# Kernel optimization log

Measured on AMD Instinct MI355X. Metric: run time of the kernel, lower is better.

Reference implementation:

```python
import jax, jax.numpy as jnp
import numpy as np
import math

SCALES = (1, 2, 4)
GROUPS = 8
EPS = 1e-5
TEMPERATURE = 1.0


def bilinear_resize(x, out_h, out_w):
    # torch F.interpolate mode='bilinear', align_corners=False
    B, C, h, w = x.shape
    def coords(out, in_):
        c = (jnp.arange(out, dtype=x.dtype) + 0.5) * (in_ / out) - 0.5
        c = jnp.clip(c, 0.0, in_ - 1.0)
        i0 = jnp.floor(c).astype(jnp.int32)
        i1 = jnp.minimum(i0 + 1, in_ - 1)
        t = c - i0.astype(x.dtype)
        return i0, i1, t
    y0, y1, ty = coords(out_h, h)
    x0, x1, tx = coords(out_w, w)
    r0 = x[:, :, y0, :]
    r1 = x[:, :, y1, :]
    v00 = r0[:, :, :, x0]; v01 = r0[:, :, :, x1]
    v10 = r1[:, :, :, x0]; v11 = r1[:, :, :, x1]
    top = v00 * (1.0 - tx) + v01 * tx
    bot = v10 * (1.0 - tx) + v11 * tx
    return top * (1.0 - ty)[:, None] + bot * ty[:, None]


def group_norm(x, gamma, beta):
    B, C, H, W = x.shape
    xg = x.reshape(B, GROUPS, C // GROUPS, H, W)
    mu = xg.mean(axis=(2, 3, 4), keepdims=True)
    var = xg.var(axis=(2, 3, 4), keepdims=True)
    xn = ((xg - mu) * jax.lax.rsqrt(var + EPS)).reshape(B, C, H, W)
    return xn * gamma[None, :, None, None] + beta[None, :, None, None]


def setup_inputs() -> dict:
    key = jax.random.key(0)
    B, C, H, W = 4, 128, 64, 64
    inter = max(C // 4, 8)  # 32
    S = len(SCALES)
    ks = jax.random.split(key, 8)
    def xavier(k, shape, fan_in, fan_out):
        a = math.sqrt(6.0 / (fan_in + fan_out))
        return jax.random.uniform(k, shape, jnp.float32, -a, a)
    inp = {
        'x': jax.random.normal(ks[0], (B, C, H, W), jnp.float32),
        'gn_w': jnp.ones((S, C), jnp.float32),
        'gn_b': jnp.zeros((S, C), jnp.float32),
        'qw': xavier(ks[1], (S, inter, C), C, inter),
        'qb': jnp.zeros((S, inter), jnp.float32),
        'kw': xavier(ks[2], (S, inter, C), C, inter),
        'kb': jnp.zeros((S, inter), jnp.float32),
        'vw': xavier(ks[3], (S, inter, C), C, inter),
        'vb': jnp.zeros((S, inter), jnp.float32),
        'ow': xavier(ks[4], (S, C, inter), inter, C),
        'ob': jnp.zeros((S, C), jnp.float32),
        'gamma': jnp.full((S,), 0.1 / S, jnp.float32),
        'scale_weights': jnp.full((S,), 1.0 / S, jnp.float32),
    }
    return inp


def _forward(x, gn_w, gn_b, qw, qb, kw, kb, vw, vb, ow, ob, gamma, scale_weights):
    B, C, H, W = x.shape
    inter = qw.shape[1]
    inv_scale = 1.0 / (TEMPERATURE * math.sqrt(inter))
    outs = []
    for i, s in enumerate(SCALES):
        if s == 1:
            xs = x
        else:
            xs = x.reshape(B, C, H // s, s, W // s, s).mean(axis=(3, 5))
        h, w = xs.shape[2], xs.shape[3]
        N = h * w
        xn = group_norm(xs, gn_w[i], gn_b[i])
        # 1x1 convs as channel contractions
        q = (jnp.einsum('oc,bchw->bohw', qw[i], xn) + qb[i][None, :, None, None]).reshape(B, inter, N)
        k = (jnp.einsum('oc,bchw->bohw', kw[i], xn) + kb[i][None, :, None, None]).reshape(B, inter, N)
        v = (jnp.einsum('oc,bchw->bohw', vw[i], xn) + vb[i][None, :, None, None]).reshape(B, inter, N)
        logits = jnp.einsum('bin,bim->bnm', q, k) * inv_scale  # [B, N, N]
        attn = jax.nn.softmax(logits, axis=-1)
        att = jnp.einsum('bnm,bim->bin', attn, v).reshape(B, inter, h, w)
        o = jnp.einsum('ci,bihw->bchw', ow[i], att) + ob[i][None, :, None, None]
        y = gamma[i] * o + xs
        if s > 1:
            y = bilinear_resize(y, H, W)
        outs.append(y)
    wts = jax.nn.softmax(scale_weights, axis=0)
    fused = wts[0] * outs[0]
    for i in range(1, len(outs)):
        fused = fused + wts[i] * outs[i]
    return fused


def reference(x, gn_w, gn_b, qw, qb, kw, kb, vw, vb, ow, ob, gamma, scale_weights):
    return _forward(x, gn_w, gn_b, qw, qb, kw, kb, vw, vb, ow, ob, gamma, scale_weights)
```

## Files before the change

### kernel.cpp

```cpp
#include <hip/hip_runtime.h>
#include <math.h>

#define B 4
#define C 128
#define G 8
#define CPG 16
#define INTER 32
#define SPLIT 16
#define KS 4

#define N1 4096
#define N2 1024
#define N4 256

#define QOFF2 (B * N1 * 32)
#define QOFF4 (QOFF2 + B * N2 * 32)
#define QTOT  (QOFF4 + B * N4 * 32)
#define PAOFF2 (B * KS * 32 * N1)
#define PAOFF4 (PAOFF2 + B * KS * 32 * N2)
#define PATOT  (PAOFF4 + B * KS * 32 * N4)
#define PMOFF2 (B * KS * 2 * N1)
#define PMOFF4 (PMOFF2 + B * KS * 2 * N2)
#define PMTOT  (PMOFF4 + B * KS * 2 * N4)

typedef unsigned short ushort_t;
typedef __attribute__((ext_vector_type(8))) short short8;
typedef __attribute__((ext_vector_type(4))) short short4v;
typedef __attribute__((ext_vector_type(4))) float f32x4;

__device__ __forceinline__ ushort_t f2bf(float f) {
    union { float f; unsigned u; } x; x.f = f;
    unsigned r = x.u + 0x7fffu + ((x.u >> 16) & 1u);
    return (ushort_t)(r >> 16);
}

__device__ __forceinline__ void scale_wts(const float* __restrict__ sw,
                                          float& w0, float& w1, float& w2) {
    float a = sw[0], b = sw[1], c = sw[2];
    float m = fmaxf(a, fmaxf(b, c));
    float e0 = __expf(a - m), e1 = __expf(b - m), e2 = __expf(c - m);
    float inv = 1.0f / (e0 + e1 + e2);
    w0 = e0 * inv; w1 = e1 * inv; w2 = e2 * inv;
}

__device__ __forceinline__ void block_reduce_write(float s, float q,
                                                   float* __restrict__ dst2) {
    __shared__ float rs[256], rq[256];
    rs[threadIdx.x] = s; rq[threadIdx.x] = q;
    __syncthreads();
    for (int st = 128; st > 0; st >>= 1) {
        if (threadIdx.x < st) {
            rs[threadIdx.x] += rs[threadIdx.x + st];
            rq[threadIdx.x] += rq[threadIdx.x + st];
        }
        __syncthreads();
    }
    if (threadIdx.x == 0) { dst2[0] = rs[0]; dst2[1] = rq[0]; }
}

__global__ __launch_bounds__(256) void pool_stats_kernel(const float* __restrict__ x,
                                                         float* __restrict__ xs2,
                                                         float* __restrict__ xs4,
                                                         float* __restrict__ part) {
    int bid = blockIdx.x;
    if (bid < 512) {
        int sp = bid & 15, bg = bid >> 4;
        const float* base = x + ((bg * CPG) << 12) + sp * 4096;
        float s = 0.0f, q = 0.0f;
        for (int i = threadIdx.x; i < 4096; i += 256) {
            float v = base[i];
            s += v; q += v * v;
        }
        block_reduce_write(s, q, part + bid * 2);
    } else if (bid < 1024) {
        int blk = bid - 512;
        int sp = blk & 15, bg = blk >> 4;
        int bc = bg * CPG + sp;
        const float* src = x + (bc << 12);
        float* dst = xs2 + (bc << 10);
        float s = 0.0f, q = 0.0f;
        for (int p = threadIdx.x; p < 1024; p += 256) {
            int oy = p >> 5, ox = p & 31;
            const float* s2 = src + oy * 128 + ox * 2;
            float v = (s2[0] + s2[1] + s2[64] + s2[65]) * 0.25f;
            dst[p] = v; s += v; q += v * v;
        }
        block_reduce_write(s, q, part + 1024 + blk * 2);
    } else {
        int blk = bid - 1024;
        int sp = blk & 15, bg = blk >> 4;
        int bc = bg * CPG + sp;
        const float* src = x + (bc << 12);
        float* dst = xs4 + (bc << 8);
        float s = 0.0f, q = 0.0f;
        if (threadIdx.x < 256) {
            int p = threadIdx.x;
            int oy = p >> 4, ox = p & 15;
            const float* s4 = src + oy * 256 + ox * 4;
            float v = 0.0f;
            #pragma unroll
            for (int dy = 0; dy < 4; ++dy)
                #pragma unroll
                for (int dx = 0; dx < 4; ++dx) v += s4[dy * 64 + dx];
            v *= 0.0625f;
            dst[p] = v; s = v; q = v * v;
        }
        block_reduce_write(s, q, part + 2048 + blk * 2);
    }
}

template <int N, int NSH>
__device__ __forceinline__ void qkv_body(int bi, const float* __restrict__ xs,
    const float* __restrict__ part,
    const float* __restrict__ gn_w, const float* __restrict__ gn_b,
    const float* __restrict__ qw, const float* __restrict__ qb,
    const float* __restrict__ kw, const float* __restrict__ kb,
    const float* __restrict__ vw, const float* __restrict__ vb,
    ushort_t* __restrict__ q_bf, ushort_t* __restrict__ k_bf, ushort_t* __restrict__ v_bf) {
    const int nc = N >> 8;
    int nchunk = bi % nc; bi /= nc;
    int og = bi & 3; bi >>= 2;
    int proj = bi % 3; int b = bi / 3;
    const float* wp = (proj == 0) ? qw : ((proj == 1) ? kw : vw);
    const float* bp = (proj == 0) ? qb : ((proj == 1) ? kb : vb);
    __shared__ float wl[8 * 128];
    __shared__ float2 ss[128];
    {
        int t = threadIdx.x;
        #pragma unroll
        for (int r = 0; r < 4; ++r) {
            int e = r * 256 + t;
            int o = e >> 7, c0 = e & 127;
            wl[c0 * 8 + o] = wp[(og * 8 + o) * C + c0];
        }
        if (t < 128) {
            int c = t;
            int bg = b * 8 + (c >> 4);
            float s = 0.0f, q = 0.0f;
            #pragma unroll
            for (int sp = 0; sp < SPLIT; ++sp) {
                s += part[(bg * SPLIT + sp) * 2];
                q += part[(bg * SPLIT + sp) * 2 + 1];
            }
            float inv = 1.0f / (float)(CPG << NSH);
            float mu = s * inv;
            float var = q * inv - mu * mu;
            float rsig = rsqrtf(var + 1e-5f);
            float a = rsig * gn_w[c];
            float2 r; r.x = a; r.y = gn_b[c] - mu * a;
            ss[c] = r;
        }
    }
    __syncthreads();
    int n = nchunk * 256 + threadIdx.x;
    const float* xb = xs + ((size_t)(b * C) << NSH) + n;
    float acc[8];
    #pragma unroll
    for (int o = 0; o < 8; ++o) acc[o] = bp[og * 8 + o];
    #pragma unroll 2
    for (int c0 = 0; c0 < C; ++c0) {
        float raw = xb[(size_t)c0 << NSH];
        float2 s2 = ss[c0];
        float xv = fmaf(s2.x, raw, s2.y);
        const float4* wr = (const float4*)&wl[c0 * 8];
        float4 w0 = wr[0], w1 = wr[1];
        acc[0] += w0.x * xv; acc[1] += w0.y * xv; acc[2] += w0.z * xv; acc[3] += w0.w * xv;
        acc[4] += w1.x * xv; acc[5] += w1.y * xv; acc[6] += w1.z * xv; acc[7] += w1.w * xv;
    }
    if (proj < 2) {
        ushort_t tmp[8];
        #pragma unroll
        for (int o = 0; o < 8; ++o) tmp[o] = f2bf(acc[o]);
        ushort_t* dst = ((proj == 0) ? q_bf : k_bf) + ((size_t)(b * N + n)) * 32 + og * 8;
        *(uint4*)dst = *(const uint4*)tmp;
    } else {
        #pragma unroll
        for (int o = 0; o < 8; ++o)
            v_bf[((size_t)(b * 32 + og * 8 + o) << NSH) + n] = f2bf(acc[o]);
    }
}

__global__ __launch_bounds__(256) void qkv_all_kernel(const float* __restrict__ x,
    const float* __restrict__ xs2, const float* __restrict__ xs4,
    const float* __restrict__ part,
    const float* __restrict__ gn_w, const float* __restrict__ gn_b,
    const float* __restrict__ qw, const float* __restrict__ qb,
    const float* __restrict__ kw, const float* __restrict__ kb,
    const float* __restrict__ vw, const float* __restrict__ vb,
    ushort_t* __restrict__ qbf, ushort_t* __restrict__ kbf, ushort_t* __restrict__ vbf) {
    int bid = blockIdx.x;
    if (bid < 768) {
        qkv_body<N1, 12>(bid, x, part, gn_w, gn_b, qw, qb, kw, kb, vw, vb, qbf, kbf, vbf);
    } else if (bid < 960) {
        qkv_body<N2, 10>(bid - 768, xs2, part + 1024, gn_w + C, gn_b + C,
                         qw + INTER * C, qb + INTER, kw + INTER * C, kb + INTER,
                         vw + INTER * C, vb + INTER,
                         qbf + QOFF2, kbf + QOFF2, vbf + QOFF2);
    } else {
        qkv_body<N4, 8>(bid - 960, xs4, part + 2048, gn_w + 2 * C, gn_b + 2 * C,
                        qw + 2 * INTER * C, qb + 2 * INTER, kw + 2 * INTER * C, kb + 2 * INTER,
                        vw + 2 * INTER * C, vb + 2 * INTER,
                        qbf + QOFF4, kbf + QOFF4, vbf + QOFF4);
    }
}

template <int N, int NSH>
__device__ __forceinline__ void attn_body(int bi,
    const ushort_t* __restrict__ q_bf, const ushort_t* __restrict__ k_bf,
    const ushort_t* __restrict__ v_bf,
    float* __restrict__ pacc, float* __restrict__ pml,
    ushort_t* K_lds, ushort_t* V_lds, ushort_t* P_lds) {
    int ks = bi % KS; bi /= KS;
    const int nqc = N >> 6;
    int qc = bi % nqc; int b = bi / nqc;
    int tid = threadIdx.x;
    int l = tid & 63, w = tid >> 6, lq = l & 15, g = l >> 4;
    int q0 = qc * 64 + w * 16;
    const float invs = 0.17677669529663687f;

    short8 qf = *(const short8*)(q_bf + ((size_t)(b * N + q0 + lq)) * 32 + g * 8);
    f32x4 acco0 = {0.f, 0.f, 0.f, 0.f}, acco1 = {0.f, 0.f, 0.f, 0.f};
    float mrun = -3.0e38f, lrun = 0.0f;

    const int kchunk = N / KS;
    int kbase = ks * kchunk;
    const int ntiles = kchunk >> 6;
    ushort_t* Pw = P_lds + w * 16 * 72;

    for (int t = 0; t < ntiles; ++t) {
        int kt0 = kbase + t * 64;
        __syncthreads();
        {
            const uint4* ksrc = (const uint4*)(k_bf + ((size_t)(b * N + kt0 + (tid >> 2))) * 32 + (tid & 3) * 8);
            *(uint4*)&K_lds[(tid >> 2) * 40 + (tid & 3) * 8] = *ksrc;
            const uint4* vsrc = (const uint4*)(v_bf + (((size_t)(b * 32 + (tid >> 3))) << NSH) + kt0 + (tid & 7) * 8);
            *(uint4*)&V_lds[(tid >> 3) * 72 + (tid & 7) * 8] = *vsrc;
        }
        __syncthreads();

        f32x4 sa[4];
        #pragma unroll
        for (int kt = 0; kt < 4; ++kt) {
            short8 kf = *(const short8*)&K_lds[(kt * 16 + lq) * 40 + g * 8];
            f32x4 z = {0.f, 0.f, 0.f, 0.f};
            sa[kt] = __builtin_amdgcn_mfma_f32_16x16x32_bf16(kf, qf, z, 0, 0, 0);
        }
        float sc[16];
        #pragma unroll
        for (int kt = 0; kt < 4; ++kt) {
            sc[kt * 4 + 0] = sa[kt][0] * invs;
            sc[kt * 4 + 1] = sa[kt][1] * invs;
            sc[kt * 4 + 2] = sa[kt][2] * invs;
            sc[kt * 4 + 3] = sa[kt][3] * invs;
        }
        float tmax = sc[0];
        #pragma unroll
        for (int j = 1; j < 16; ++j) tmax = fmaxf(tmax, sc[j]);
        tmax = fmaxf(tmax, __shfl_xor(tmax, 16, 64));
        tmax = fmaxf(tmax, __shfl_xor(tmax, 32, 64));
        float nm = fmaxf(mrun, tmax);
        float corr = __expf(mrun - nm);
        float psum = 0.0f;
        ushort_t pb[16];
        #pragma unroll
        for (int j = 0; j < 16; ++j) {
            float p = __expf(sc[j] - nm);
            psum += p;
            pb[j] = f2bf(p);
        }
        psum += __shfl_xor(psum, 16, 64);
        psum += __shfl_xor(psum, 32, 64);
        lrun = lrun * corr + psum;
        mrun = nm;
        #pragma unroll
        for (int e = 0; e < 4; ++e) { acco0[e] *= corr; acco1[e] *= corr; }
        #pragma unroll
        for (int kt = 0; kt < 4; ++kt) {
            short4v pv4;
            pv4[0] = (short)pb[kt * 4 + 0];
            pv4[1] = (short)pb[kt * 4 + 1];
            pv4[2] = (short)pb[kt * 4 + 2];
            pv4[3] = (short)pb[kt * 4 + 3];
            *(short4v*)&Pw[lq * 72 + kt * 16 + g * 4] = pv4;
        }
        #pragma unroll
        for (int c = 0; c < 2; ++c) {
            short8 pf  = *(const short8*)&Pw[lq * 72 + c * 32 + g * 8];
            short8 vf0 = *(const short8*)&V_lds[(lq) * 72 + c * 32 + g * 8];
            short8 vf1 = *(const short8*)&V_lds[(16 + lq) * 72 + c * 32 + g * 8];
            acco0 = __builtin_amdgcn_mfma_f32_16x16x32_bf16(vf0, pf, acco0, 0, 0, 0);
            acco1 = __builtin_amdgcn_mfma_f32_16x16x32_bf16(vf1, pf, acco1, 0, 0, 0);
        }
    }
    int n = q0 + lq;
    size_t pb_ = ((size_t)(b * KS + ks)) * 32;
    #pragma unroll
    for (int r = 0; r < 4; ++r) {
        pacc[(pb_ + (g * 4 + r)) * N + n]      = acco0[r];
        pacc[(pb_ + 16 + (g * 4 + r)) * N + n] = acco1[r];
    }
    if (g == 0) {
        pml[((size_t)(b * KS + ks) * 2) * N + n]     = mrun;
        pml[((size_t)(b * KS + ks) * 2 + 1) * N + n] = lrun;
    }
}

__global__ __launch_bounds__(256) void attn_all_kernel(
    const ushort_t* __restrict__ qbf, const ushort_t* __restrict__ kbf,
    const ushort_t* __restrict__ vbf,
    float* __restrict__ pacc, float* __restrict__ pml) {
    __shared__ ushort_t K_lds[64 * 40];
    __shared__ ushort_t V_lds[32 * 72];
    __shared__ ushort_t P_lds[4 * 16 * 72];
    int bid = blockIdx.x;
    if (bid < 1024) {
        attn_body<N1, 12>(bid, qbf, kbf, vbf, pacc, pml, K_lds, V_lds, P_lds);
    } else if (bid < 1280) {
        attn_body<N2, 10>(bid - 1024, qbf + QOFF2, kbf + QOFF2, vbf + QOFF2,
                          pacc + PAOFF2, pml + PMOFF2, K_lds, V_lds, P_lds);
    } else {
        attn_body<N4, 8>(bid - 1280, qbf + QOFF4, kbf + QOFF4, vbf + QOFF4,
                         pacc + PAOFF4, pml + PMOFF4, K_lds, V_lds, P_lds);
    }
}

template <int N, int NSH>
__device__ __forceinline__ void comb_oy_body(int tile, const float* __restrict__ pacc,
                                             const float* __restrict__ pml,
                                             const float* __restrict__ ow,
                                             const float* __restrict__ ob,
                                             const float* __restrict__ gamma,
                                             const float* __restrict__ xs,
                                             float* __restrict__ ydst,
                                             const float* __restrict__ sw,
                                             float* att_lds, float* ow_lds) {
    const int ntiles = N >> 5;
    int b = tile / ntiles;
    int n0 = (tile % ntiles) << 5;
    int t = threadIdx.x;
    {
        const float4* src = (const float4*)ow;
        float4* dst = (float4*)ow_lds;
        dst[t] = src[t];
        dst[256 + t] = src[256 + t];
        dst[512 + t] = src[512 + t];
        dst[768 + t] = src[768 + t];
    }
    {
        int o = t >> 3, j = t & 3, half = (t >> 2) & 1;
        o = t >> 3; j = t & 7;
        int n = n0 + j * 4;
        float4 mv[KS], lv[KS], av[KS];
        float4 M = {-3.0e38f, -3.0e38f, -3.0e38f, -3.0e38f};
        #pragma unroll
        for (int ks = 0; ks < KS; ++ks) {
            mv[ks] = *(const float4*)&pml[((size_t)(b * KS + ks) * 2) * N + n];
            lv[ks] = *(const float4*)&pml[((size_t)(b * KS + ks) * 2 + 1) * N + n];
            av[ks] = *(const float4*)&pacc[((size_t)(b * KS + ks) * INTER + o) * N + n];
            M.x = fmaxf(M.x, mv[ks].x); M.y = fmaxf(M.y, mv[ks].y);
            M.z = fmaxf(M.z, mv[ks].z); M.w = fmaxf(M.w, mv[ks].w);
        }
        float4 L = {0.f, 0.f, 0.f, 0.f}, A = {0.f, 0.f, 0.f, 0.f};
        #pragma unroll
        for (int ks = 0; ks < KS; ++ks) {
            float4 wgt;
            wgt.x = __expf(mv[ks].x - M.x); wgt.y = __expf(mv[ks].y - M.y);
            wgt.z = __expf(mv[ks].z - M.z); wgt.w = __expf(mv[ks].w - M.w);
            L.x += lv[ks].x * wgt.x; L.y += lv[ks].y * wgt.y;
            L.z += lv[ks].z * wgt.z; L.w += lv[ks].w * wgt.w;
            A.x += av[ks].x * wgt.x; A.y += av[ks].y * wgt.y;
            A.z += av[ks].z * wgt.z; A.w += av[ks].w * wgt.w;
        }
        float4 r;
        r.x = A.x / L.x; r.y = A.y / L.y; r.z = A.z / L.z; r.w = A.w / L.w;
        *(float4*)&att_lds[o * 36 + j * 4] = r;
    }
    __syncthreads();
    {
        int n = t & 31;
        int cg = t >> 5;
        float av[INTER];
        #pragma unroll
        for (int i = 0; i < INTER; ++i) av[i] = att_lds[i * 36 + n];
        float gm = gamma[0];
        float wsc = 1.0f;
        bool scale = (sw != nullptr);
        if (scale) { float w0, w1, w2; scale_wts(sw, w0, w1, w2); wsc = w0; }
        const float* xsb = xs + ((size_t)(b * C + cg * 16) << NSH) + n0 + n;
        float* yb = ydst + ((size_t)(b * C + cg * 16) << NSH) + n0 + n;
        #pragma unroll
        for (int cc = 0; cc < 16; ++cc) {
            int c = cg * 16 + cc;
            const float4* wr = (const float4*)&ow_lds[c * 32];
            float a0 = 0.f, a1 = 0.f, a2 = 0.f, a3 = 0.f;
            #pragma unroll
            for (int i4 = 0; i4 < 8; ++i4) {
                float4 wv = wr[i4];
                a0 += wv.x * av[i4 * 4 + 0];
                a1 += wv.y * av[i4 * 4 + 1];
                a2 += wv.z * av[i4 * 4 + 2];
                a3 += wv.w * av[i4 * 4 + 3];
            }
            float o = ob[c] + ((a0 + a1) + (a2 + a3));
            float y = gm * o + xsb[(size_t)cc << NSH];
            yb[(size_t)cc << NSH] = wsc * y;
        }
    }
}

__global__ __launch_bounds__(256) void comb_oy_all_kernel(const float* __restrict__ pacc,
    const float* __restrict__ pml,
    const float* __restrict__ ow, const float* __restrict__ ob,
    const float* __restrict__ gamma,
    const float* __restrict__ x, const float* __restrict__ xs2, const float* __restrict__ xs4,
    float* __restrict__ out, float* __restrict__ y2, float* __restrict__ y4,
    const float* __restrict__ sw) {
    __shared__ float att_lds[32 * 36];
    __shared__ float ow_lds[128 * 32];
    int bid = blockIdx.x;
    if (bid < 512) {
        comb_oy_body<N1, 12>(bid, pacc, pml, ow, ob, gamma, x, out, sw, att_lds, ow_lds);
    } else if (bid < 640) {
        comb_oy_body<N2, 10>(bid - 512, pacc + PAOFF2, pml + PMOFF2,
                             ow + C * INTER, ob + C, gamma + 1, xs2, y2, nullptr,
                             att_lds, ow_lds);
    } else {
        comb_oy_body<N4, 8>(bid - 640, pacc + PAOFF4, pml + PMOFF4,
                            ow + 2 * C * INTER, ob + 2 * C, gamma + 2, xs4, y4, nullptr,
                            att_lds, ow_lds);
    }
}

__device__ __forceinline__ float bilerp(const float* __restrict__ img, int in,
                                        int oy, int ox, float r) {
    float cy = (oy + 0.5f) * r - 0.5f;
    cy = fminf(fmaxf(cy, 0.0f), (float)(in - 1));
    float cx = (ox + 0.5f) * r - 0.5f;
    cx = fminf(fmaxf(cx, 0.0f), (float)(in - 1));
    int y0 = (int)cy; int y1i = (y0 + 1 < in) ? y0 + 1 : in - 1; float ty = cy - (float)y0;
    int x0 = (int)cx; int x1i = (x0 + 1 < in) ? x0 + 1 : in - 1; float tx = cx - (float)x0;
    float v00 = img[y0 * in + x0];
    float v01 = img[y0 * in + x1i];
    float v10 = img[y1i * in + x0];
    float v11 = img[y1i * in + x1i];
    float top = v00 * (1.0f - tx) + v01 * tx;
    float bot = v10 * (1.0f - tx) + v11 * tx;
    return top * (1.0f - ty) + bot * ty;
}

__global__ __launch_bounds__(256) void fuse_kernel(float* __restrict__ out,
                                                   const float* __restrict__ y2,
                                                   const float* __restrict__ y4,
                                                   const float* __restrict__ sw) {
    int idx = blockIdx.x * 256 + threadIdx.x;
    int p = idx & 4095;
    int bc = idx >> 12;
    int oy = p >> 6, ox = p & 63;
    float w0, w1, w2; scale_wts(sw, w0, w1, w2);
    float v2 = bilerp(y2 + bc * 1024, 32, oy, ox, 0.5f);
    float v4 = bilerp(y4 + bc * 256, 16, oy, ox, 0.25f);
    out[idx] = out[idx] + w1 * v2 + w2 * v4;
}

extern "C" void kernel_launch(void* const* d_in, const int* in_sizes, int n_in,
                              void* d_out, int out_size, void* d_ws, size_t ws_size,
                              hipStream_t stream) {
    const float* x     = (const float*)d_in[0];
    const float* gn_w  = (const float*)d_in[1];
    const float* gn_b  = (const float*)d_in[2];
    const float* qw    = (const float*)d_in[3];
    const float* qb    = (const float*)d_in[4];
    const float* kw    = (const float*)d_in[5];
    const float* kb    = (const float*)d_in[6];
    const float* vw    = (const float*)d_in[7];
    const float* vb    = (const float*)d_in[8];
    const float* ow    = (const float*)d_in[9];
    const float* ob    = (const float*)d_in[10];
    const float* gamma = (const float*)d_in[11];
    const float* sw    = (const float*)d_in[12];
    float* out = (float*)d_out;

    float* ws    = (float*)d_ws;
    float* xs2   = ws;
    float* xs4   = xs2 + 524288;
    float* y2    = xs4 + 131072;
    float* y4    = y2 + 524288;
    float* part  = y4 + 131072;
    float* pacc  = part + 3072;
    float* pml   = pacc + PATOT;
    ushort_t* qbf = (ushort_t*)(pml + PMTOT);
    ushort_t* kbf = qbf + QTOT;
    ushort_t* vbf = kbf + QTOT;

    pool_stats_kernel<<<1536, 256, 0, stream>>>(x, xs2, xs4, part);
    qkv_all_kernel<<<1008, 256, 0, stream>>>(x, xs2, xs4, part, gn_w, gn_b,
                                             qw, qb, kw, kb, vw, vb, qbf, kbf, vbf);
    attn_all_kernel<<<1344, 256, 0, stream>>>(qbf, kbf, vbf, pacc, pml);
    comb_oy_all_kernel<<<672, 256, 0, stream>>>(pacc, pml, ow, ob, gamma,
                                                x, xs2, xs4, out, y2, y4, sw);
    fuse_kernel<<<8192, 256, 0, stream>>>(out, y2, y4, sw);
}
```

Measured before the change: 81.76 us.

## Merge all stages into one cooperative persistent kernel with grid syncs

Replaces the five separate kernel launches with a single cooperative kernel that runs each stage in a grid-stride loop, separated by grid-wide syncs. The stages are also rescheduled: the QKV projection now computes all 32 outputs per thread from pre-transposed weights, the small-scale attentions run before the full-resolution one, the small-scale combine overlaps with full-resolution attention, and the final bilinear fuse is folded into the full-scale combine. The aim is to remove launch gaps and intermediate round trips. The cost is grid.sync overhead, occupancy-limited grid size, and higher register pressure from 32 accumulators.

```diff
diff --git a/kernel.cpp b/kernel.cpp
--- a/kernel.cpp
+++ b/kernel.cpp
@@ -1,9 +1,11 @@
 #include <hip/hip_runtime.h>
+#include <hip/hip_cooperative_groups.h>
 #include <math.h>
+
+namespace cg = cooperative_groups;
 
 #define B 4
 #define C 128
-#define G 8
 #define CPG 16
 #define INTER 32
 #define SPLIT 16
@@ -23,6 +25,8 @@
 #define PMOFF4 (PMOFF2 + B * KS * 2 * N2)
 #define PMTOT  (PMOFF4 + B * KS * 2 * N4)
 
+#define SMEM_BYTES 20992
+
 typedef unsigned short ushort_t;
 typedef __attribute__((ext_vector_type(8))) short short8;
 typedef __attribute__((ext_vector_type(4))) short short4v;
@@ -43,9 +47,10 @@
     w0 = e0 * inv; w1 = e1 * inv; w2 = e2 * inv;
 }
 
-__device__ __forceinline__ void block_reduce_write(float s, float q,
+__device__ __forceinline__ void block_reduce_write(char* smem, float s, float q,
                                                    float* __restrict__ dst2) {
-    __shared__ float rs[256], rq[256];
+    float* rs = (float*)smem;
+    float* rq = rs + 256;
     rs[threadIdx.x] = s; rq[threadIdx.x] = q;
     __syncthreads();
     for (int st = 128; st > 0; st >>= 1) {
@@ -56,24 +61,26 @@
         __syncthreads();
     }
     if (threadIdx.x == 0) { dst2[0] = rs[0]; dst2[1] = rq[0]; }
-}
-
-__global__ __launch_bounds__(256) void pool_stats_kernel(const float* __restrict__ x,
-                                                         float* __restrict__ xs2,
-                                                         float* __restrict__ xs4,
-                                                         float* __restrict__ part) {
-    int bid = blockIdx.x;
-    if (bid < 512) {
-        int sp = bid & 15, bg = bid >> 4;
+    __syncthreads();
+}
+
+__device__ __forceinline__ void phase1_body(int wb, const float* __restrict__ x,
+                                            float* __restrict__ xs2, float* __restrict__ xs4,
+                                            float* __restrict__ part, float* __restrict__ wT,
+                                            const float* __restrict__ qw,
+                                            const float* __restrict__ kw,
+                                            const float* __restrict__ vw, char* smem) {
+    if (wb < 512) {
+        int sp = wb & 15, bg = wb >> 4;
         const float* base = x + ((bg * CPG) << 12) + sp * 4096;
         float s = 0.0f, q = 0.0f;
         for (int i = threadIdx.x; i < 4096; i += 256) {
             float v = base[i];
             s += v; q += v * v;
         }
-        block_reduce_write(s, q, part + bid * 2);
-    } else if (bid < 1024) {
-        int blk = bid - 512;
+        block_reduce_write(smem, s, q, part + wb * 2);
+    } else if (wb < 1024) {
+        int blk = wb - 512;
         int sp = blk & 15, bg = blk >> 4;
         int bc = bg * CPG + sp;
         const float* src = x + (bc << 12);
@@ -85,131 +92,106 @@
             float v = (s2[0] + s2[1] + s2[64] + s2[65]) * 0.25f;
             dst[p] = v; s += v; q += v * v;
         }
-        block_reduce_write(s, q, part + 1024 + blk * 2);
-    } else {
-        int blk = bid - 1024;
+        block_reduce_write(smem, s, q, part + 1024 + blk * 2);
+    } else if (wb < 1536) {
+        int blk = wb - 1024;
         int sp = blk & 15, bg = blk >> 4;
         int bc = bg * CPG + sp;
         const float* src = x + (bc << 12);
         float* dst = xs4 + (bc << 8);
+        int p = threadIdx.x & 255;
+        int oy = p >> 4, ox = p & 15;
+        const float* s4 = src + oy * 256 + ox * 4;
+        float v = 0.0f;
+        #pragma unroll
+        for (int dy = 0; dy < 4; ++dy)
+            #pragma unroll
+            for (int dx = 0; dx < 4; ++dx) v += s4[dy * 64 + dx];
+        v *= 0.0625f;
+        dst[p] = v;
+        block_reduce_write(smem, v, v * v, part + 2048 + blk * 2);
+    } else {
+        int u = wb - 1536;
+        int si = u / 3, proj = u % 3;
+        const float* src = ((proj == 0) ? qw : (proj == 1) ? kw : vw) + si * INTER * C;
+        float* dst = wT + (si * 3 + proj) * (INTER * C);
+        int t = threadIdx.x;
+        #pragma unroll
+        for (int r = 0; r < 16; ++r) {
+            int e = r * 256 + t;
+            int c = e >> 5, o = e & 31;
+            dst[e] = src[o * C + c];
+        }
+        __syncthreads();
+    }
+}
+
+template <int N, int NSH>
+__device__ __forceinline__ void qkv_body2(int proj, int b, int nchunk,
+    const float* __restrict__ xs, const float* __restrict__ part,
+    const float* __restrict__ gn_w, const float* __restrict__ gn_b,
+    const float* __restrict__ wT, const float* __restrict__ bp,
+    ushort_t* __restrict__ q_bf, ushort_t* __restrict__ k_bf, ushort_t* __restrict__ v_bf,
+    char* smem) {
+    float2* ss = (float2*)smem;
+    int t = threadIdx.x;
+    if (t < 128) {
+        int c = t, bg = b * 8 + (c >> 4);
         float s = 0.0f, q = 0.0f;
-        if (threadIdx.x < 256) {
-            int p = threadIdx.x;
-            int oy = p >> 4, ox = p & 15;
-            const float* s4 = src + oy * 256 + ox * 4;
-            float v = 0.0f;
-            #pragma unroll
-            for (int dy = 0; dy < 4; ++dy)
-                #pragma unroll
-                for (int dx = 0; dx < 4; ++dx) v += s4[dy * 64 + dx];
-            v *= 0.0625f;
-            dst[p] = v; s = v; q = v * v;
-        }
-        block_reduce_write(s, q, part + 2048 + blk * 2);
-    }
-}
-
-template <int N, int NSH>
-__device__ __forceinline__ void qkv_body(int bi, const float* __restrict__ xs,
-    const float* __restrict__ part,
-    const float* __restrict__ gn_w, const float* __restrict__ gn_b,
-    const float* __restrict__ qw, const float* __restrict__ qb,
-    const float* __restrict__ kw, const float* __restrict__ kb,
-    const float* __restrict__ vw, const float* __restrict__ vb,
-    ushort_t* __restrict__ q_bf, ushort_t* __restrict__ k_bf, ushort_t* __restrict__ v_bf) {
-    const int nc = N >> 8;
-    int nchunk = bi % nc; bi /= nc;
-    int og = bi & 3; bi >>= 2;
-    int proj = bi % 3; int b = bi / 3;
-    const float* wp = (proj == 0) ? qw : ((proj == 1) ? kw : vw);
-    const float* bp = (proj == 0) ? qb : ((proj == 1) ? kb : vb);
-    __shared__ float wl[8 * 128];
-    __shared__ float2 ss[128];
-    {
-        int t = threadIdx.x;
-        #pragma unroll
-        for (int r = 0; r < 4; ++r) {
-            int e = r * 256 + t;
-            int o = e >> 7, c0 = e & 127;
-            wl[c0 * 8 + o] = wp[(og * 8 + o) * C + c0];
-        }
-        if (t < 128) {
-            int c = t;
-            int bg = b * 8 + (c >> 4);
-            float s = 0.0f, q = 0.0f;
-            #pragma unroll
-            for (int sp = 0; sp < SPLIT; ++sp) {
-                s += part[(bg * SPLIT + sp) * 2];
-                q += part[(bg * SPLIT + sp) * 2 + 1];
-            }
-            float inv = 1.0f / (float)(CPG << NSH);
-            float mu = s * inv;
-            float var = q * inv - mu * mu;
-            float rsig = rsqrtf(var + 1e-5f);
-            float a = rsig * gn_w[c];
-            float2 r; r.x = a; r.y = gn_b[c] - mu * a;
-            ss[c] = r;
-        }
-    }
-    __syncthreads();
-    int n = nchunk * 256 + threadIdx.x;
+        #pragma unroll
+        for (int sp = 0; sp < SPLIT; ++sp) {
+            s += part[(bg * SPLIT + sp) * 2];
+            q += part[(bg * SPLIT + sp) * 2 + 1];
+        }
+        float inv = 1.0f / (float)(CPG << NSH);
+        float mu = s * inv;
+        float var = q * inv - mu * mu;
+        float a = rsqrtf(var + 1e-5f) * gn_w[c];
+        float2 r; r.x = a; r.y = gn_b[c] - mu * a;
+        ss[c] = r;
+    }
+    __syncthreads();
+    int n = nchunk * 256 + t;
     const float* xb = xs + ((size_t)(b * C) << NSH) + n;
-    float acc[8];
+    float acc[32];
     #pragma unroll
-    for (int o = 0; o < 8; ++o) acc[o] = bp[og * 8 + o];
+    for (int o = 0; o < 32; ++o) acc[o] = bp[o];
     #pragma unroll 2
     for (int c0 = 0; c0 < C; ++c0) {
-        float raw = xb[(size_t)c0 << NSH];
         float2 s2 = ss[c0];
-        float xv = fmaf(s2.x, raw, s2.y);
-        const float4* wr = (const float4*)&wl[c0 * 8];
-        float4 w0 = wr[0], w1 = wr[1];
-        acc[0] += w0.x * xv; acc[1] += w0.y * xv; acc[2] += w0.z * xv; acc[3] += w0.w * xv;
-        acc[4] += w1.x * xv; acc[5] += w1.y * xv; acc[6] += w1.z * xv; acc[7] += w1.w * xv;
+        float xv = fmaf(s2.x, xb[(size_t)c0 << NSH], s2.y);
+        const float4* wr = (const float4*)&wT[c0 * 32];
+        #pragma unroll
+        for (int i4 = 0; i4 < 8; ++i4) {
+            float4 wv = wr[i4];
+            acc[i4 * 4 + 0] += wv.x * xv; acc[i4 * 4 + 1] += wv.y * xv;
+            acc[i4 * 4 + 2] += wv.z * xv; acc[i4 * 4 + 3] += wv.w * xv;
+        }
     }
     if (proj < 2) {
-        ushort_t tmp[8];
-        #pragma unroll
-        for (int o = 0; o < 8; ++o) tmp[o] = f2bf(acc[o]);
-        ushort_t* dst = ((proj == 0) ? q_bf : k_bf) + ((size_t)(b * N + n)) * 32 + og * 8;
-        *(uint4*)dst = *(const uint4*)tmp;
+        ushort_t tmp[32];
+        #pragma unroll
+        for (int o = 0; o < 32; ++o) tmp[o] = f2bf(acc[o]);
+        ushort_t* dst = ((proj == 0) ? q_bf : k_bf) + (size_t)(b * N + n) * 32;
+        const uint4* tv = (const uint4*)tmp;
+        ((uint4*)dst)[0] = tv[0]; ((uint4*)dst)[1] = tv[1];
+        ((uint4*)dst)[2] = tv[2]; ((uint4*)dst)[3] = tv[3];
     } else {
         #pragma unroll
-        for (int o = 0; o < 8; ++o)
-            v_bf[((size_t)(b * 32 + og * 8 + o) << NSH) + n] = f2bf(acc[o]);
-    }
-}
-
-__global__ __launch_bounds__(256) void qkv_all_kernel(const float* __restrict__ x,
-    const float* __restrict__ xs2, const float* __restrict__ xs4,
-    const float* __restrict__ part,
-    const float* __restrict__ gn_w, const float* __restrict__ gn_b,
-    const float* __restrict__ qw, const float* __restrict__ qb,
-    const float* __restrict__ kw, const float* __restrict__ kb,
-    const float* __restrict__ vw, const float* __restrict__ vb,
-    ushort_t* __restrict__ qbf, ushort_t* __restrict__ kbf, ushort_t* __restrict__ vbf) {
-    int bid = blockIdx.x;
-    if (bid < 768) {
-        qkv_body<N1, 12>(bid, x, part, gn_w, gn_b, qw, qb, kw, kb, vw, vb, qbf, kbf, vbf);
-    } else if (bid < 960) {
-        qkv_body<N2, 10>(bid - 768, xs2, part + 1024, gn_w + C, gn_b + C,
-                         qw + INTER * C, qb + INTER, kw + INTER * C, kb + INTER,
-                         vw + INTER * C, vb + INTER,
-                         qbf + QOFF2, kbf + QOFF2, vbf + QOFF2);
-    } else {
-        qkv_body<N4, 8>(bid - 960, xs4, part + 2048, gn_w + 2 * C, gn_b + 2 * C,
-                        qw + 2 * INTER * C, qb + 2 * INTER, kw + 2 * INTER * C, kb + 2 * INTER,
-                        vw + 2 * INTER * C, vb + 2 * INTER,
-                        qbf + QOFF4, kbf + QOFF4, vbf + QOFF4);
-    }
+        for (int o = 0; o < 32; ++o)
+            v_bf[((size_t)(b * 32 + o) << NSH) + n] = f2bf(acc[o]);
+    }
+    __syncthreads();
 }
 
 template <int N, int NSH>
 __device__ __forceinline__ void attn_body(int bi,
     const ushort_t* __restrict__ q_bf, const ushort_t* __restrict__ k_bf,
     const ushort_t* __restrict__ v_bf,
-    float* __restrict__ pacc, float* __restrict__ pml,
-    ushort_t* K_lds, ushort_t* V_lds, ushort_t* P_lds) {
+    float* __restrict__ pacc, float* __restrict__ pml, char* smem) {
+    ushort_t* K_lds = (ushort_t*)smem;
+    ushort_t* V_lds = (ushort_t*)(smem + 5120);
+    ushort_t* P_lds = (ushort_t*)(smem + 9728);
     int ks = bi % KS; bi /= KS;
     const int nqc = N >> 6;
     int qc = bi % nqc; int b = bi / nqc;
@@ -303,37 +285,16 @@
         pml[((size_t)(b * KS + ks) * 2) * N + n]     = mrun;
         pml[((size_t)(b * KS + ks) * 2 + 1) * N + n] = lrun;
     }
-}
-
-__global__ __launch_bounds__(256) void attn_all_kernel(
-    const ushort_t* __restrict__ qbf, const ushort_t* __restrict__ kbf,
-    const ushort_t* __restrict__ vbf,
-    float* __restrict__ pacc, float* __restrict__ pml) {
-    __shared__ ushort_t K_lds[64 * 40];
-    __shared__ ushort_t V_lds[32 * 72];
-    __shared__ ushort_t P_lds[4 * 16 * 72];
-    int bid = blockIdx.x;
-    if (bid < 1024) {
-        attn_body<N1, 12>(bid, qbf, kbf, vbf, pacc, pml, K_lds, V_lds, P_lds);
-    } else if (bid < 1280) {
-        attn_body<N2, 10>(bid - 1024, qbf + QOFF2, kbf + QOFF2, vbf + QOFF2,
-                          pacc + PAOFF2, pml + PMOFF2, K_lds, V_lds, P_lds);
-    } else {
-        attn_body<N4, 8>(bid - 1280, qbf + QOFF4, kbf + QOFF4, vbf + QOFF4,
-                         pacc + PAOFF4, pml + PMOFF4, K_lds, V_lds, P_lds);
-    }
+    __syncthreads();
 }
 
 template <int N, int NSH>
 __device__ __forceinline__ void comb_oy_body(int tile, const float* __restrict__ pacc,
-                                             const float* __restrict__ pml,
-                                             const float* __restrict__ ow,
-                                             const float* __restrict__ ob,
-                                             const float* __restrict__ gamma,
-                                             const float* __restrict__ xs,
-                                             float* __restrict__ ydst,
-                                             const float* __restrict__ sw,
-                                             float* att_lds, float* ow_lds) {
+    const float* __restrict__ pml, const float* __restrict__ ow, const float* __restrict__ ob,
+    const float* __restrict__ gamma, const float* __restrict__ xs,
+    float* __restrict__ ydst, char* smem) {
+    float* att_lds = (float*)smem;
+    float* ow_lds  = (float*)(smem + 4608);
     const int ntiles = N >> 5;
     int b = tile / ntiles;
     int n0 = (tile % ntiles) << 5;
@@ -341,35 +302,32 @@
     {
         const float4* src = (const float4*)ow;
         float4* dst = (float4*)ow_lds;
-        dst[t] = src[t];
-        dst[256 + t] = src[256 + t];
-        dst[512 + t] = src[512 + t];
-        dst[768 + t] = src[768 + t];
+        dst[t] = src[t]; dst[256 + t] = src[256 + t];
+        dst[512 + t] = src[512 + t]; dst[768 + t] = src[768 + t];
     }
     {
-        int o = t >> 3, j = t & 3, half = (t >> 2) & 1;
-        o = t >> 3; j = t & 7;
+        int o = t >> 3, j = t & 7;
         int n = n0 + j * 4;
-        float4 mv[KS], lv[KS], av[KS];
+        float4 mv[KS], lv[KS], av4[KS];
         float4 M = {-3.0e38f, -3.0e38f, -3.0e38f, -3.0e38f};
         #pragma unroll
-        for (int ks = 0; ks < KS; ++ks) {
-            mv[ks] = *(const float4*)&pml[((size_t)(b * KS + ks) * 2) * N + n];
-            lv[ks] = *(const float4*)&pml[((size_t)(b * KS + ks) * 2 + 1) * N + n];
-            av[ks] = *(const float4*)&pacc[((size_t)(b * KS + ks) * INTER + o) * N + n];
-            M.x = fmaxf(M.x, mv[ks].x); M.y = fmaxf(M.y, mv[ks].y);
-            M.z = fmaxf(M.z, mv[ks].z); M.w = fmaxf(M.w, mv[ks].w);
+        for (int k2 = 0; k2 < KS; ++k2) {
+            mv[k2]  = *(const float4*)&pml[((size_t)(b * KS + k2) * 2) * N + n];
+            lv[k2]  = *(const float4*)&pml[((size_t)(b * KS + k2) * 2 + 1) * N + n];
+            av4[k2] = *(const float4*)&pacc[((size_t)(b * KS + k2) * INTER + o) * N + n];
+            M.x = fmaxf(M.x, mv[k2].x); M.y = fmaxf(M.y, mv[k2].y);
+            M.z = fmaxf(M.z, mv[k2].z); M.w = fmaxf(M.w, mv[k2].w);
         }
         float4 L = {0.f, 0.f, 0.f, 0.f}, A = {0.f, 0.f, 0.f, 0.f};
         #pragma unroll
-        for (int ks = 0; ks < KS; ++ks) {
-            float4 wgt;
-            wgt.x = __expf(mv[ks].x - M.x); wgt.y = __expf(mv[ks].y - M.y);
-            wgt.z = __expf(mv[ks].z - M.z); wgt.w = __expf(mv[ks].w - M.w);
-            L.x += lv[ks].x * wgt.x; L.y += lv[ks].y * wgt.y;
-            L.z += lv[ks].z * wgt.z; L.w += lv[ks].w * wgt.w;
-            A.x += av[ks].x * wgt.x; A.y += av[ks].y * wgt.y;
-            A.z += av[ks].z * wgt.z; A.w += av[ks].w * wgt.w;
+        for (int k2 = 0; k2 < KS; ++k2) {
+            float4 wg;
+            wg.x = __expf(mv[k2].x - M.x); wg.y = __expf(mv[k2].y - M.y);
+            wg.z = __expf(mv[k2].z - M.z); wg.w = __expf(mv[k2].w - M.w);
+            L.x += lv[k2].x * wg.x; L.y += lv[k2].y * wg.y;
+            L.z += lv[k2].z * wg.z; L.w += lv[k2].w * wg.w;
+            A.x += av4[k2].x * wg.x; A.y += av4[k2].y * wg.y;
+            A.z += av4[k2].z * wg.z; A.w += av4[k2].w * wg.w;
         }
         float4 r;
         r.x = A.x / L.x; r.y = A.y / L.y; r.z = A.z / L.z; r.w = A.w / L.w;
@@ -377,89 +335,193 @@
     }
     __syncthreads();
     {
-        int n = t & 31;
-        int cg = t >> 5;
-        float av[INTER];
-        #pragma unroll
-        for (int i = 0; i < INTER; ++i) av[i] = att_lds[i * 36 + n];
+        int n = t & 31, cg2 = t >> 5;
+        float av[32];
+        #pragma unroll
+        for (int i = 0; i < 32; ++i) av[i] = att_lds[i * 36 + n];
         float gm = gamma[0];
-        float wsc = 1.0f;
-        bool scale = (sw != nullptr);
-        if (scale) { float w0, w1, w2; scale_wts(sw, w0, w1, w2); wsc = w0; }
-        const float* xsb = xs + ((size_t)(b * C + cg * 16) << NSH) + n0 + n;
-        float* yb = ydst + ((size_t)(b * C + cg * 16) << NSH) + n0 + n;
-        #pragma unroll
+        const float* xsb = xs + ((size_t)(b * C + cg2 * 16) << NSH) + n0 + n;
+        float* yb = ydst + ((size_t)(b * C + cg2 * 16) << NSH) + n0 + n;
+        #pragma unroll 4
         for (int cc = 0; cc < 16; ++cc) {
-            int c = cg * 16 + cc;
+            int c = cg2 * 16 + cc;
             const float4* wr = (const float4*)&ow_lds[c * 32];
             float a0 = 0.f, a1 = 0.f, a2 = 0.f, a3 = 0.f;
             #pragma unroll
             for (int i4 = 0; i4 < 8; ++i4) {
                 float4 wv = wr[i4];
-                a0 += wv.x * av[i4 * 4 + 0];
-                a1 += wv.y * av[i4 * 4 + 1];
-                a2 += wv.z * av[i4 * 4 + 2];
-                a3 += wv.w * av[i4 * 4 + 3];
+                a0 += wv.x * av[i4 * 4 + 0]; a1 += wv.y * av[i4 * 4 + 1];
+                a2 += wv.z * av[i4 * 4 + 2]; a3 += wv.w * av[i4 * 4 + 3];
             }
-            float o = ob[c] + ((a0 + a1) + (a2 + a3));
-            float y = gm * o + xsb[(size_t)cc << NSH];
-            yb[(size_t)cc << NSH] = wsc * y;
-        }
-    }
-}
-
-__global__ __launch_bounds__(256) void comb_oy_all_kernel(const float* __restrict__ pacc,
-    const float* __restrict__ pml,
+            float o_ = ob[c] + ((a0 + a1) + (a2 + a3));
+            yb[(size_t)cc << NSH] = gm * o_ + xsb[(size_t)cc << NSH];
+        }
+    }
+    __syncthreads();
+}
+
+__device__ __forceinline__ void comb_oy_s1_fuse_body(int tile,
+    const float* __restrict__ pacc, const float* __restrict__ pml,
     const float* __restrict__ ow, const float* __restrict__ ob,
-    const float* __restrict__ gamma,
-    const float* __restrict__ x, const float* __restrict__ xs2, const float* __restrict__ xs4,
-    float* __restrict__ out, float* __restrict__ y2, float* __restrict__ y4,
-    const float* __restrict__ sw) {
-    __shared__ float att_lds[32 * 36];
-    __shared__ float ow_lds[128 * 32];
-    int bid = blockIdx.x;
-    if (bid < 512) {
-        comb_oy_body<N1, 12>(bid, pacc, pml, ow, ob, gamma, x, out, sw, att_lds, ow_lds);
-    } else if (bid < 640) {
-        comb_oy_body<N2, 10>(bid - 512, pacc + PAOFF2, pml + PMOFF2,
-                             ow + C * INTER, ob + C, gamma + 1, xs2, y2, nullptr,
-                             att_lds, ow_lds);
-    } else {
-        comb_oy_body<N4, 8>(bid - 640, pacc + PAOFF4, pml + PMOFF4,
-                            ow + 2 * C * INTER, ob + 2 * C, gamma + 2, xs4, y4, nullptr,
-                            att_lds, ow_lds);
-    }
-}
-
-__device__ __forceinline__ float bilerp(const float* __restrict__ img, int in,
-                                        int oy, int ox, float r) {
-    float cy = (oy + 0.5f) * r - 0.5f;
-    cy = fminf(fmaxf(cy, 0.0f), (float)(in - 1));
-    float cx = (ox + 0.5f) * r - 0.5f;
-    cx = fminf(fmaxf(cx, 0.0f), (float)(in - 1));
-    int y0 = (int)cy; int y1i = (y0 + 1 < in) ? y0 + 1 : in - 1; float ty = cy - (float)y0;
-    int x0 = (int)cx; int x1i = (x0 + 1 < in) ? x0 + 1 : in - 1; float tx = cx - (float)x0;
-    float v00 = img[y0 * in + x0];
-    float v01 = img[y0 * in + x1i];
-    float v10 = img[y1i * in + x0];
-    float v11 = img[y1i * in + x1i];
-    float top = v00 * (1.0f - tx) + v01 * tx;
-    float bot = v10 * (1.0f - tx) + v11 * tx;
-    return top * (1.0f - ty) + bot * ty;
-}
-
-__global__ __launch_bounds__(256) void fuse_kernel(float* __restrict__ out,
-                                                   const float* __restrict__ y2,
-                                                   const float* __restrict__ y4,
-                                                   const float* __restrict__ sw) {
-    int idx = blockIdx.x * 256 + threadIdx.x;
-    int p = idx & 4095;
-    int bc = idx >> 12;
-    int oy = p >> 6, ox = p & 63;
-    float w0, w1, w2; scale_wts(sw, w0, w1, w2);
-    float v2 = bilerp(y2 + bc * 1024, 32, oy, ox, 0.5f);
-    float v4 = bilerp(y4 + bc * 256, 16, oy, ox, 0.25f);
-    out[idx] = out[idx] + w1 * v2 + w2 * v4;
+    const float* __restrict__ gamma, const float* __restrict__ x,
+    const float* __restrict__ y2, const float* __restrict__ y4,
+    float* __restrict__ out, const float* __restrict__ sw, char* smem) {
+    float* att_lds = (float*)smem;
+    float* ow_lds  = (float*)(smem + 4608);
+    const int N = N1;
+    int b = tile >> 7;
+    int n0 = (tile & 127) << 5;
+    int t = threadIdx.x;
+    {
+        const float4* src = (const float4*)ow;
+        float4* dst = (float4*)ow_lds;
+        dst[t] = src[t]; dst[256 + t] = src[256 + t];
+        dst[512 + t] = src[512 + t]; dst[768 + t] = src[768 + t];
+    }
+    {
+        int o = t >> 3, j = t & 7;
+        int n = n0 + j * 4;
+        float4 mv[KS], lv[KS], av4[KS];
+        float4 M = {-3.0e38f, -3.0e38f, -3.0e38f, -3.0e38f};
+        #pragma unroll
+        for (int k2 = 0; k2 < KS; ++k2) {
+            mv[k2]  = *(const float4*)&pml[((size_t)(b * KS + k2) * 2) * N + n];
+            lv[k2]  = *(const float4*)&pml[((size_t)(b * KS + k2) * 2 + 1) * N + n];
+            av4[k2] = *(const float4*)&pacc[((size_t)(b * KS + k2) * INTER + o) * N + n];
+            M.x = fmaxf(M.x, mv[k2].x); M.y = fmaxf(M.y, mv[k2].y);
+            M.z = fmaxf(M.z, mv[k2].z); M.w = fmaxf(M.w, mv[k2].w);
+        }
+        float4 L = {0.f, 0.f, 0.f, 0.f}, A = {0.f, 0.f, 0.f, 0.f};
+        #pragma unroll
+        for (int k2 = 0; k2 < KS; ++k2) {
+            float4 wg;
+            wg.x = __expf(mv[k2].x - M.x); wg.y = __expf(mv[k2].y - M.y);
+            wg.z = __expf(mv[k2].z - M.z); wg.w = __expf(mv[k2].w - M.w);
+            L.x += lv[k2].x * wg.x; L.y += lv[k2].y * wg.y;
+            L.z += lv[k2].z * wg.z; L.w += lv[k2].w * wg.w;
+            A.x += av4[k2].x * wg.x; A.y += av4[k2].y * wg.y;
+            A.z += av4[k2].z * wg.z; A.w += av4[k2].w * wg.w;
+        }
+        float4 r;
+        r.x = A.x / L.x; r.y = A.y / L.y; r.z = A.z / L.z; r.w = A.w / L.w;
+        *(float4*)&att_lds[o * 36 + j * 4] = r;
+    }
+    __syncthreads();
+    {
+        int n = t & 31, cg2 = t >> 5;
+        float av[32];
+        #pragma unroll
+        for (int i = 0; i < 32; ++i) av[i] = att_lds[i * 36 + n];
+        float gm = gamma[0];
+        float w0, w1, w2; scale_wts(sw, w0, w1, w2);
+        int p = n0 + n, oy = p >> 6, ox = p & 63;
+        float cy2 = fminf(fmaxf((oy + 0.5f) * 0.5f - 0.5f, 0.0f), 31.0f);
+        int ya0 = (int)cy2; int ya1 = (ya0 + 1 < 32) ? ya0 + 1 : 31; float ty2 = cy2 - (float)ya0;
+        float cx2 = fminf(fmaxf((ox + 0.5f) * 0.5f - 0.5f, 0.0f), 31.0f);
+        int xa0 = (int)cx2; int xa1 = (xa0 + 1 < 32) ? xa0 + 1 : 31; float tx2 = cx2 - (float)xa0;
+        float cy4 = fminf(fmaxf((oy + 0.5f) * 0.25f - 0.5f, 0.0f), 15.0f);
+        int yb0 = (int)cy4; int yb1 = (yb0 + 1 < 16) ? yb0 + 1 : 15; float ty4 = cy4 - (float)yb0;
+        float cx4 = fminf(fmaxf((ox + 0.5f) * 0.25f - 0.5f, 0.0f), 15.0f);
+        int xb0 = (int)cx4; int xb1 = (xb0 + 1 < 16) ? xb0 + 1 : 15; float tx4 = cx4 - (float)xb0;
+        const float* xsb = x + ((size_t)(b * C + cg2 * 16) << 12) + p;
+        float* outp = out + ((size_t)(b * C + cg2 * 16) << 12) + p;
+        const float* y2b = y2 + (size_t)(b * C + cg2 * 16) * 1024;
+        const float* y4b = y4 + (size_t)(b * C + cg2 * 16) * 256;
+        #pragma unroll 4
+        for (int cc = 0; cc < 16; ++cc) {
+            int c = cg2 * 16 + cc;
+            const float4* wr = (const float4*)&ow_lds[c * 32];
+            float a0 = 0.f, a1 = 0.f, a2 = 0.f, a3 = 0.f;
+            #pragma unroll
+            for (int i4 = 0; i4 < 8; ++i4) {
+                float4 wv = wr[i4];
+                a0 += wv.x * av[i4 * 4 + 0]; a1 += wv.y * av[i4 * 4 + 1];
+                a2 += wv.z * av[i4 * 4 + 2]; a3 += wv.w * av[i4 * 4 + 3];
+            }
+            float o_ = ob[c] + ((a0 + a1) + (a2 + a3));
+            float yv = gm * o_ + xsb[(size_t)cc << 12];
+            const float* i2 = y2b + cc * 1024;
+            float top2 = i2[ya0 * 32 + xa0] * (1.f - tx2) + i2[ya0 * 32 + xa1] * tx2;
+            float bot2 = i2[ya1 * 32 + xa0] * (1.f - tx2) + i2[ya1 * 32 + xa1] * tx2;
+            float v2 = top2 * (1.f - ty2) + bot2 * ty2;
+            const float* i4p = y4b + cc * 256;
+            float top4 = i4p[yb0 * 16 + xb0] * (1.f - tx4) + i4p[yb0 * 16 + xb1] * tx4;
+            float bot4 = i4p[yb1 * 16 + xb0] * (1.f - tx4) + i4p[yb1 * 16 + xb1] * tx4;
+            float v4 = top4 * (1.f - ty4) + bot4 * ty4;
+            outp[(size_t)cc << 12] = w0 * yv + w1 * v2 + w2 * v4;
+        }
+    }
+    __syncthreads();
+}
+
+__global__ __launch_bounds__(256) void msa_mega_kernel(
+    const float* __restrict__ x, const float* __restrict__ gn_w, const float* __restrict__ gn_b,
+    const float* __restrict__ qw, const float* __restrict__ qb,
+    const float* __restrict__ kw, const float* __restrict__ kb,
+    const float* __restrict__ vw, const float* __restrict__ vb,
+    const float* __restrict__ ow, const float* __restrict__ ob,
+    const float* __restrict__ gamma, const float* __restrict__ sw,
+    float* __restrict__ out,
+    float* __restrict__ xs2, float* __restrict__ xs4,
+    float* __restrict__ y2, float* __restrict__ y4,
+    float* __restrict__ part, float* __restrict__ wT,
+    float* __restrict__ pacc, float* __restrict__ pml,
+    ushort_t* __restrict__ qbf, ushort_t* __restrict__ kbf, ushort_t* __restrict__ vbf) {
+    extern __shared__ char smem[];
+    cg::grid_group grid = cg::this_grid();
+    const int gsz = gridDim.x;
+
+    for (int wb = blockIdx.x; wb < 1545; wb += gsz)
+        phase1_body(wb, x, xs2, xs4, part, wT, qw, kw, vw, smem);
+    grid.sync();
+
+    for (int wb = blockIdx.x; wb < 252; wb += gsz) {
+        if (wb < 192) {
+            int proj = wb / 64, r = wb % 64, b_ = r >> 4, nch = r & 15;
+            qkv_body2<N1, 12>(proj, b_, nch, x, part, gn_w, gn_b,
+                wT + proj * (INTER * C),
+                ((proj == 0) ? qb : (proj == 1) ? kb : vb),
+                qbf, kbf, vbf, smem);
+        } else if (wb < 240) {
+            int u = wb - 192, proj = u / 16, r = u % 16, b_ = r >> 2, nch = r & 3;
+            qkv_body2<N2, 10>(proj, b_, nch, xs2, part + 1024, gn_w + C, gn_b + C,
+                wT + (3 + proj) * (INTER * C),
+                ((proj == 0) ? qb : (proj == 1) ? kb : vb) + INTER,
+                qbf + QOFF2, kbf + QOFF2, vbf + QOFF2, smem);
+        } else {
+            int u = wb - 240, proj = u / 4, b_ = u % 4;
+            qkv_body2<N4, 8>(proj, b_, 0, xs4, part + 2048, gn_w + 2 * C, gn_b + 2 * C,
+                wT + (6 + proj) * (INTER * C),
+                ((proj == 0) ? qb : (proj == 1) ? kb : vb) + 2 * INTER,
+                qbf + QOFF4, kbf + QOFF4, vbf + QOFF4, smem);
+        }
+    }
+    grid.sync();
+
+    for (int wb = blockIdx.x; wb < 320; wb += gsz) {
+        if (wb < 256)
+            attn_body<N2, 10>(wb, qbf + QOFF2, kbf + QOFF2, vbf + QOFF2,
+                              pacc + PAOFF2, pml + PMOFF2, smem);
+        else
+            attn_body<N4, 8>(wb - 256, qbf + QOFF4, kbf + QOFF4, vbf + QOFF4,
+                             pacc + PAOFF4, pml + PMOFF4, smem);
+    }
+    grid.sync();
+
+    for (int wb = blockIdx.x; wb < 1184; wb += gsz) {
+        if (wb < 1024)
+            attn_body<N1, 12>(wb, qbf, kbf, vbf, pacc, pml, smem);
+        else if (wb < 1152)
+            comb_oy_body<N2, 10>(wb - 1024, pacc + PAOFF2, pml + PMOFF2,
+                                 ow + C * INTER, ob + C, gamma + 1, xs2, y2, smem);
+        else
+            comb_oy_body<N4, 8>(wb - 1152, pacc + PAOFF4, pml + PMOFF4,
+                                ow + 2 * C * INTER, ob + 2 * C, gamma + 2, xs4, y4, smem);
+    }
+    grid.sync();
+
+    for (int wb = blockIdx.x; wb < 512; wb += gsz)
+        comb_oy_s1_fuse_body(wb, pacc, pml, ow, ob, gamma, x, y2, y4, out, sw, smem);
 }
 
 extern "C" void kernel_launch(void* const* d_in, const int* in_sizes, int n_in,
@@ -486,17 +548,26 @@
     float* y2    = xs4 + 131072;
     float* y4    = y2 + 524288;
     float* part  = y4 + 131072;
-    float* pacc  = part + 3072;
+    float* wT    = part + 3072;
+    float* pacc  = wT + 36864;
     float* pml   = pacc + PATOT;
     ushort_t* qbf = (ushort_t*)(pml + PMTOT);
     ushort_t* kbf = qbf + QTOT;
     ushort_t* vbf = kbf + QTOT;
 
-    pool_stats_kernel<<<1536, 256, 0, stream>>>(x, xs2, xs4, part);
-    qkv_all_kernel<<<1008, 256, 0, stream>>>(x, xs2, xs4, part, gn_w, gn_b,
-                                             qw, qb, kw, kb, vw, vb, qbf, kbf, vbf);
-    attn_all_kernel<<<1344, 256, 0, stream>>>(qbf, kbf, vbf, pacc, pml);
-    comb_oy_all_kernel<<<672, 256, 0, stream>>>(pacc, pml, ow, ob, gamma,
-                                                x, xs2, xs4, out, y2, y4, sw);
-    fuse_kernel<<<8192, 256, 0, stream>>>(out, y2, y4, sw);
-}
+    int maxb = 0;
+    hipOccupancyMaxActiveBlocksPerMultiprocessor(&maxb, (const void*)msa_mega_kernel,
+                                                 256, (size_t)SMEM_BYTES);
+    if (maxb < 1) maxb = 1;
+    int grid = maxb * 256;
+    if (grid > 1184) grid = 1184;
+
+    void* kargs[] = { (void*)&x, (void*)&gn_w, (void*)&gn_b, (void*)&qw, (void*)&qb,
+                      (void*)&kw, (void*)&kb, (void*)&vw, (void*)&vb, (void*)&ow,
+                      (void*)&ob, (void*)&gamma, (void*)&sw, (void*)&out,
+                      (void*)&xs2, (void*)&xs4, (void*)&y2, (void*)&y4,
+                      (void*)&part, (void*)&wT, (void*)&pacc, (void*)&pml,
+                      (void*)&qbf, (void*)&kbf, (void*)&vbf };
+    hipLaunchCooperativeKernel((void*)msa_mega_kernel, dim3(grid), dim3(256),
+                               kargs, SMEM_BYTES, stream);
+}
```

Measured after the change: 291.2 us. +256.1%, slower.
